# Optimization experiments

Hardware: AMD Instinct MI355X
Metric: run time of the kernel (lower is better)

## Reference

```python
import jax, jax.numpy as jnp
from jax import lax
import numpy as np

D_MODEL = 256
EXPAND = 2
D_INNER = D_MODEL * EXPAND
B, T = 8, 4096


def setup_inputs() -> dict:
    key = jax.random.key(0)
    ks = jax.random.split(key, 7)
    s_lin = 1.0 / np.sqrt(D_MODEL)
    s_gru_i = 1.0 / np.sqrt(D_MODEL)  # torch GRU init: U(-1/sqrt(hidden), 1/sqrt(hidden))
    x = jax.random.normal(ks[0], (B, T, D_MODEL), dtype=jnp.float32)
    W1 = jax.random.uniform(ks[1], (D_INNER, D_MODEL), jnp.float32, -s_lin, s_lin)
    b1 = jax.random.uniform(ks[2], (D_INNER,), jnp.float32, -s_lin, s_lin)
    W_ih = jax.random.uniform(ks[3], (3 * D_MODEL, D_INNER), jnp.float32, -s_gru_i, s_gru_i)
    b_ih = jax.random.uniform(ks[4], (3 * D_MODEL,), jnp.float32, -s_gru_i, s_gru_i)
    W_hh = jax.random.uniform(ks[5], (3 * D_MODEL, D_MODEL), jnp.float32, -s_gru_i, s_gru_i)
    b_hh = jax.random.uniform(ks[6], (3 * D_MODEL,), jnp.float32, -s_gru_i, s_gru_i)
    return {"x": x, "W1": W1, "b1": b1, "W_ih": W_ih, "b_ih": b_ih, "W_hh": W_hh, "b_hh": b_hh}


def reference(x, W1, b1, W_ih, b_ih, W_hh, b_hh):
    # Linear(d_model -> d_inner) + exact GELU (torch default)
    h = jax.nn.gelu(jnp.einsum('btd,id->bti', x, W1) + b1, approximate=False)  # [B,T,Di]
    Bb, Tt, _ = h.shape
    H = W_hh.shape[1]
    # Precompute input-side gate pre-activations for all timesteps (order: r, z, n)
    gx = jnp.einsum('bti,gi->btg', h, W_ih) + b_ih  # [B,T,3H]
    gx = jnp.moveaxis(gx, 1, 0)                     # [T,B,3H]

    def step(hprev, g):
        gh = hprev @ W_hh.T + b_hh                  # [B,3H]
        xr, xz, xn = jnp.split(g, 3, axis=-1)
        hr, hz, hn = jnp.split(gh, 3, axis=-1)
        r = jax.nn.sigmoid(xr + hr)
        z = jax.nn.sigmoid(xz + hz)
        n = jnp.tanh(xn + r * hn)
        hnew = (1.0 - z) * n + z * hprev
        return hnew, hnew

    h0 = jnp.zeros((Bb, H), dtype=x.dtype)
    _, out = lax.scan(step, h0, gx)                 # out: [T,B,H]
    return jnp.moveaxis(out, 0, 1)                  # [B,T,H]
```

## Files before the change

kernel.cpp:

```cpp
#include <hip/hip_runtime.h>
#include <hip/hip_fp16.h>
#include <hip/hip_bf16.h>

#define DM   256
#define DI   512
#define TG   768
#define TSEQ 4096
#define NB   8
#define MTOT (NB*TSEQ)

typedef _Float16 h2f __attribute__((ext_vector_type(2)));
typedef _Float16 h8f __attribute__((ext_vector_type(8)));

template<bool A_HALF, bool GELU_ACT>
__global__ __launch_bounds__(256) void gemm_bias(
    const void* __restrict__ Ap, const float* __restrict__ W,
    const float* __restrict__ bias, __half* __restrict__ C,
    int M, int N, int K)
{
  __shared__ float As[16][132];
  __shared__ float Ws[16][132];
  const int tid = threadIdx.x;
  const int tx = tid & 15, ty = tid >> 4;
  const int m0 = blockIdx.y * 128;
  const int n0 = blockIdx.x * 128;

  float acc[8][8] = {};

  for (int k0 = 0; k0 < K; k0 += 16) {
    if constexpr (A_HALF) {
      const __half* A = (const __half*)Ap;
      int r = tid >> 1, seg = (tid & 1) * 8;
      float4 raw = *(const float4*)(A + (size_t)(m0 + r) * K + k0 + seg);
      const __half* hv = (const __half*)&raw;
      #pragma unroll
      for (int q = 0; q < 8; q++) As[seg + q][r] = __half2float(hv[q]);
    } else {
      const float* A = (const float*)Ap;
      #pragma unroll
      for (int rep = 0; rep < 2; rep++) {
        int r = (tid >> 2) + rep * 64;
        int seg = (tid & 3) * 4;
        float4 v = *(const float4*)(A + (size_t)(m0 + r) * K + k0 + seg);
        As[seg + 0][r] = v.x; As[seg + 1][r] = v.y;
        As[seg + 2][r] = v.z; As[seg + 3][r] = v.w;
      }
    }
    #pragma unroll
    for (int rep = 0; rep < 2; rep++) {
      int r = (tid >> 2) + rep * 64;
      int seg = (tid & 3) * 4;
      float4 v = *(const float4*)(W + (size_t)(n0 + r) * K + k0 + seg);
      Ws[seg + 0][r] = v.x; Ws[seg + 1][r] = v.y;
      Ws[seg + 2][r] = v.z; Ws[seg + 3][r] = v.w;
    }
    __syncthreads();
    #pragma unroll
    for (int kk = 0; kk < 16; ++kk) {
      float a[8], b[8];
      *(float4*)&a[0] = *(const float4*)&As[kk][ty * 8];
      *(float4*)&a[4] = *(const float4*)&As[kk][ty * 8 + 4];
      *(float4*)&b[0] = *(const float4*)&Ws[kk][tx * 8];
      *(float4*)&b[4] = *(const float4*)&Ws[kk][tx * 8 + 4];
      #pragma unroll
      for (int i = 0; i < 8; i++)
        #pragma unroll
        for (int j = 0; j < 8; j++)
          acc[i][j] += a[i] * b[j];
    }
    __syncthreads();
  }

  #pragma unroll
  for (int i = 0; i < 8; i++) {
    int m = m0 + ty * 8 + i;
    #pragma unroll
    for (int j = 0; j < 8; j++) {
      int n = n0 + tx * 8 + j;
      float v = acc[i][j] + bias[n];
      if constexpr (GELU_ACT) {
        v = 0.5f * v * (1.0f + erff(v * 0.70710678118654752f));
      }
      C[(size_t)m * N + n] = __float2half(v);
    }
  }
}

__global__ __launch_bounds__(768, 3) void gru_scan(
    const __half* __restrict__ gx,
    const float*  __restrict__ Whh,
    const float*  __restrict__ bhh,
    float* __restrict__ out)
{
  const int b = blockIdx.x;
  const int j = threadIdx.x;

  __shared__ __align__(16) _Float16 h16[DM];
  __shared__ float gsig[2 * DM];

  h2f w[128];
  const float* wrow = Whh + (size_t)j * DM;
  #pragma unroll
  for (int k4 = 0; k4 < 64; k4++) {
    float4 f = ((const float4*)wrow)[k4];
    h2f t0; t0[0] = (_Float16)f.x; t0[1] = (_Float16)f.y;
    h2f t1; t1[0] = (_Float16)f.z; t1[1] = (_Float16)f.w;
    w[2 * k4]     = t0;
    w[2 * k4 + 1] = t1;
  }
  const float bias = bhh[j];
  float hloc = 0.0f;

  if (j < DM) h16[j] = (_Float16)0.0f;
  __syncthreads();

  const __half* gxb = gx + (size_t)b * TSEQ * TG;
  float* outb = out + (size_t)b * TSEQ * DM;

  float gxv = __half2float(gxb[j]);

  for (int t = 0; t < TSEQ; ++t) {
    float a0 = bias, a1 = 0.f, a2 = 0.f, a3 = 0.f;
    const h8f* hp8 = (const h8f*)h16;
    #pragma unroll
    for (int k = 0; k < 32; k++) {
      union { h8f v; h2f p[4]; } u;
      u.v = hp8[k];
      a0 = __builtin_amdgcn_fdot2(w[4 * k + 0], u.p[0], a0, false);
      a1 = __builtin_amdgcn_fdot2(w[4 * k + 1], u.p[1], a1, false);
      a2 = __builtin_amdgcn_fdot2(w[4 * k + 2], u.p[2], a2, false);
      a3 = __builtin_amdgcn_fdot2(w[4 * k + 3], u.p[3], a3, false);
    }
    float gh = (a0 + a1) + (a2 + a3);

    float gxn = 0.f;
    if (t + 1 < TSEQ) gxn = __half2float(gxb[(size_t)(t + 1) * TG + j]);

    if (j < 2 * DM) {
      float s = 1.0f / (1.0f + __expf(-(gxv + gh)));
      gsig[j] = s;
    }
    __syncthreads();
    if (j >= 2 * DM) {
      const int i = j - 2 * DM;
      float r = gsig[i];
      float z = gsig[i + DM];
      float n = tanhf(gxv + r * gh);
      float hn = (1.0f - z) * n + z * hloc;
      hloc = hn;
      h16[i] = (_Float16)hn;
      outb[(size_t)t * DM + i] = hn;
    }
    __syncthreads();
    gxv = gxn;
  }
}

extern "C" void kernel_launch(void* const* d_in, const int* in_sizes, int n_in,
                              void* d_out, int out_size, void* d_ws, size_t ws_size,
                              hipStream_t stream) {
  const float* x   = (const float*)d_in[0];
  const float* W1  = (const float*)d_in[1];
  const float* b1  = (const float*)d_in[2];
  const float* Wih = (const float*)d_in[3];
  const float* bih = (const float*)d_in[4];
  const float* Whh = (const float*)d_in[5];
  const float* bhh = (const float*)d_in[6];
  float* out = (float*)d_out;

  char* ws = (char*)d_ws;
  __half* h  = (__half*)ws;
  size_t h_bytes = (size_t)MTOT * DI * sizeof(__half);
  h_bytes = (h_bytes + 255) & ~(size_t)255;
  __half* gxbuf = (__half*)(ws + h_bytes);

  dim3 blk(256);
  gemm_bias<false, true><<<dim3(DI / 128, MTOT / 128), blk, 0, stream>>>(
      x, W1, b1, h, MTOT, DI, DM);
  gemm_bias<true, false><<<dim3(TG / 128, MTOT / 128), blk, 0, stream>>>(
      h, Wih, bih, gxbuf, MTOT, TG, DI);
  gru_scan<<<NB, 768, 0, stream>>>(gxbuf, Whh, bhh, out);
}
```

Baseline: 5.861 ms.

## Split GRU recurrent matvec across 4-lane groups with DPP reductions

Each group of four threads now shares four W_hh rows, and each thread covers a quarter of the K dimension for all four rows, combining partial sums with DPP xor-1/xor-2 butterfly adds. Each thread then picks out the reduced value for its own row. The aim is to cut per-thread LDS reads of the hidden state by a factor of four, since each thread now reads only 64 of the 256 h values. The cost is extra DPP and select instructions, plus sched_barriers that constrain instruction scheduling.

```diff
diff --git a/kernel.cpp b/kernel.cpp
--- a/kernel.cpp
+++ b/kernel.cpp
@@ -86,27 +86,51 @@
   }
 }
 
+__device__ __forceinline__ float dpp_xor1_add(float v) {
+  int i = __builtin_bit_cast(int, v);
+  int s = __builtin_amdgcn_update_dpp(i, i, 0xB1, 0xF, 0xF, true);
+  return v + __builtin_bit_cast(float, s);
+}
+__device__ __forceinline__ float dpp_xor2_add(float v) {
+  int i = __builtin_bit_cast(int, v);
+  int s = __builtin_amdgcn_update_dpp(i, i, 0x4E, 0xF, 0xF, true);
+  return v + __builtin_bit_cast(float, s);
+}
+
 __global__ __launch_bounds__(768, 3) void gru_scan(
     const __half* __restrict__ gx,
     const float*  __restrict__ Whh,
     const float*  __restrict__ bhh,
     float* __restrict__ out)
 {
-  const int b = blockIdx.x;
-  const int j = threadIdx.x;
+  const int b  = blockIdx.x;
+  const int j  = threadIdx.x;
+  const int g  = j >> 2;
+  const int q  = j & 3;
+  const int row0 = g << 2;
 
   __shared__ __align__(16) _Float16 h16[DM];
   __shared__ float gsig[2 * DM];
 
   h2f w[128];
-  const float* wrow = Whh + (size_t)j * DM;
   #pragma unroll
-  for (int k4 = 0; k4 < 64; k4++) {
-    float4 f = ((const float4*)wrow)[k4];
-    h2f t0; t0[0] = (_Float16)f.x; t0[1] = (_Float16)f.y;
-    h2f t1; t1[0] = (_Float16)f.z; t1[1] = (_Float16)f.w;
-    w[2 * k4]     = t0;
-    w[2 * k4 + 1] = t1;
+  for (int r = 0; r < 4; ++r) {
+    const float* wrow = Whh + (size_t)(row0 + r) * DM;
+    #pragma unroll
+    for (int i = 0; i < 8; ++i) {
+      const float* p = wrow + 8 * (q + 4 * i);
+      float4 f0 = *(const float4*)(p);
+      float4 f1 = *(const float4*)(p + 4);
+      h2f t0; t0[0] = (_Float16)f0.x; t0[1] = (_Float16)f0.y;
+      h2f t1; t1[0] = (_Float16)f0.z; t1[1] = (_Float16)f0.w;
+      h2f t2; t2[0] = (_Float16)f1.x; t2[1] = (_Float16)f1.y;
+      h2f t3; t3[0] = (_Float16)f1.z; t3[1] = (_Float16)f1.w;
+      w[r * 32 + 4 * i + 0] = t0;
+      w[r * 32 + 4 * i + 1] = t1;
+      w[r * 32 + 4 * i + 2] = t2;
+      w[r * 32 + 4 * i + 3] = t3;
+      __builtin_amdgcn_sched_barrier(0);
+    }
   }
   const float bias = bhh[j];
   float hloc = 0.0f;
@@ -114,42 +138,60 @@
   if (j < DM) h16[j] = (_Float16)0.0f;
   __syncthreads();
 
-  const __half* gxb = gx + (size_t)b * TSEQ * TG;
+  const __half* gxb = gx + (size_t)b * TSEQ * TG + j;
   float* outb = out + (size_t)b * TSEQ * DM;
 
-  float gxv = __half2float(gxb[j]);
+  float gxv = __half2float(gxb[0]);
+  const h8f* hp8 = (const h8f*)h16;
 
   for (int t = 0; t < TSEQ; ++t) {
-    float a0 = bias, a1 = 0.f, a2 = 0.f, a3 = 0.f;
-    const h8f* hp8 = (const h8f*)h16;
-    #pragma unroll
-    for (int k = 0; k < 32; k++) {
+    float a0 = 0.f, a1 = 0.f, a2 = 0.f, a3 = 0.f;
+    #pragma unroll
+    for (int i = 0; i < 8; ++i) {
       union { h8f v; h2f p[4]; } u;
-      u.v = hp8[k];
-      a0 = __builtin_amdgcn_fdot2(w[4 * k + 0], u.p[0], a0, false);
-      a1 = __builtin_amdgcn_fdot2(w[4 * k + 1], u.p[1], a1, false);
-      a2 = __builtin_amdgcn_fdot2(w[4 * k + 2], u.p[2], a2, false);
-      a3 = __builtin_amdgcn_fdot2(w[4 * k + 3], u.p[3], a3, false);
-    }
-    float gh = (a0 + a1) + (a2 + a3);
+      u.v = hp8[q + 4 * i];
+      a0 = __builtin_amdgcn_fdot2(w[      4 * i + 0], u.p[0], a0, false);
+      a0 = __builtin_amdgcn_fdot2(w[      4 * i + 1], u.p[1], a0, false);
+      a0 = __builtin_amdgcn_fdot2(w[      4 * i + 2], u.p[2], a0, false);
+      a0 = __builtin_amdgcn_fdot2(w[      4 * i + 3], u.p[3], a0, false);
+      a1 = __builtin_amdgcn_fdot2(w[ 32 + 4 * i + 0], u.p[0], a1, false);
+      a1 = __builtin_amdgcn_fdot2(w[ 32 + 4 * i + 1], u.p[1], a1, false);
+      a1 = __builtin_amdgcn_fdot2(w[ 32 + 4 * i + 2], u.p[2], a1, false);
+      a1 = __builtin_amdgcn_fdot2(w[ 32 + 4 * i + 3], u.p[3], a1, false);
+      a2 = __builtin_amdgcn_fdot2(w[ 64 + 4 * i + 0], u.p[0], a2, false);
+      a2 = __builtin_amdgcn_fdot2(w[ 64 + 4 * i + 1], u.p[1], a2, false);
+      a2 = __builtin_amdgcn_fdot2(w[ 64 + 4 * i + 2], u.p[2], a2, false);
+      a2 = __builtin_amdgcn_fdot2(w[ 64 + 4 * i + 3], u.p[3], a2, false);
+      a3 = __builtin_amdgcn_fdot2(w[ 96 + 4 * i + 0], u.p[0], a3, false);
+      a3 = __builtin_amdgcn_fdot2(w[ 96 + 4 * i + 1], u.p[1], a3, false);
+      a3 = __builtin_amdgcn_fdot2(w[ 96 + 4 * i + 2], u.p[2], a3, false);
+      a3 = __builtin_amdgcn_fdot2(w[ 96 + 4 * i + 3], u.p[3], a3, false);
+      if (i & 1) __builtin_amdgcn_sched_barrier(0);
+    }
+    a0 = dpp_xor2_add(dpp_xor1_add(a0));
+    a1 = dpp_xor2_add(dpp_xor1_add(a1));
+    a2 = dpp_xor2_add(dpp_xor1_add(a2));
+    a3 = dpp_xor2_add(dpp_xor1_add(a3));
+    float lo = (q & 1) ? a1 : a0;
+    float hi = (q & 1) ? a3 : a2;
+    float gh = ((q & 2) ? hi : lo) + bias;
 
     float gxn = 0.f;
-    if (t + 1 < TSEQ) gxn = __half2float(gxb[(size_t)(t + 1) * TG + j]);
+    if (t + 1 < TSEQ) gxn = __half2float(gxb[(size_t)(t + 1) * TG]);
 
     if (j < 2 * DM) {
-      float s = 1.0f / (1.0f + __expf(-(gxv + gh)));
-      gsig[j] = s;
+      gsig[j] = 1.0f / (1.0f + __expf(-(gxv + gh)));
     }
     __syncthreads();
     if (j >= 2 * DM) {
-      const int i = j - 2 * DM;
-      float r = gsig[i];
-      float z = gsig[i + DM];
+      const int i2 = j - 2 * DM;
+      float r = gsig[i2];
+      float z = gsig[i2 + DM];
       float n = tanhf(gxv + r * gh);
       float hn = (1.0f - z) * n + z * hloc;
       hloc = hn;
-      h16[i] = (_Float16)hn;
-      outb[(size_t)t * DM + i] = hn;
+      h16[i2] = (_Float16)hn;
+      outb[(size_t)t * DM + i2] = hn;
     }
     __syncthreads();
     gxv = gxn;
```

Result: faster. 5.600 ms (-4.4%).

## Restructure GRU scan so each thread pair computes all gates for one unit

Applied to the files above, without the earlier changes.

The recurrent scan now uses 512 threads in which a pair of lanes splits the K dimension for one hidden unit and computes the r, z and n dot products together. The two halves are combined with a DPP xor-1 add. Because all gate math stays in registers, the gsig shared-memory exchange goes away, and double-buffering the hidden state cuts the per-step barriers from two to one. The cost is 192 half2 weight registers per thread, which raises register pressure.

```diff
diff --git a/kernel.cpp b/kernel.cpp
--- a/kernel.cpp
+++ b/kernel.cpp
@@ -86,7 +86,13 @@
   }
 }
 
-__global__ __launch_bounds__(768, 3) void gru_scan(
+__device__ __forceinline__ float dpp_xor1_add(float v) {
+  int i = __builtin_bit_cast(int, v);
+  int s = __builtin_amdgcn_update_dpp(i, i, 0xB1, 0xF, 0xF, true);
+  return v + __builtin_bit_cast(float, s);
+}
+
+__global__ __launch_bounds__(512, 2) void gru_scan(
     const __half* __restrict__ gx,
     const float*  __restrict__ Whh,
     const float*  __restrict__ bhh,
@@ -94,65 +100,105 @@
 {
   const int b = blockIdx.x;
   const int j = threadIdx.x;
-
-  __shared__ __align__(16) _Float16 h16[DM];
-  __shared__ float gsig[2 * DM];
-
-  h2f w[128];
-  const float* wrow = Whh + (size_t)j * DM;
-  #pragma unroll
-  for (int k4 = 0; k4 < 64; k4++) {
-    float4 f = ((const float4*)wrow)[k4];
-    h2f t0; t0[0] = (_Float16)f.x; t0[1] = (_Float16)f.y;
-    h2f t1; t1[0] = (_Float16)f.z; t1[1] = (_Float16)f.w;
-    w[2 * k4]     = t0;
-    w[2 * k4 + 1] = t1;
-  }
-  const float bias = bhh[j];
+  const int u = j >> 1;
+  const int p = j & 1;
+
+  __shared__ __align__(16) _Float16 hbuf[2][DM];
+
+  h2f wr[64], wz[64], wn[64];
+  {
+    const float* rr = Whh + (size_t)u * DM + p * 128;
+    const float* rz = rr + (size_t)DM * DM;
+    const float* rn = rz + (size_t)DM * DM;
+    #pragma unroll
+    for (int i = 0; i < 32; ++i) {
+      float4 f = *(const float4*)(rr + 4 * i);
+      h2f t0; t0[0] = (_Float16)f.x; t0[1] = (_Float16)f.y;
+      h2f t1; t1[0] = (_Float16)f.z; t1[1] = (_Float16)f.w;
+      wr[2 * i] = t0; wr[2 * i + 1] = t1;
+      if (i & 1) __builtin_amdgcn_sched_barrier(0);
+    }
+    #pragma unroll
+    for (int i = 0; i < 32; ++i) {
+      float4 f = *(const float4*)(rz + 4 * i);
+      h2f t0; t0[0] = (_Float16)f.x; t0[1] = (_Float16)f.y;
+      h2f t1; t1[0] = (_Float16)f.z; t1[1] = (_Float16)f.w;
+      wz[2 * i] = t0; wz[2 * i + 1] = t1;
+      if (i & 1) __builtin_amdgcn_sched_barrier(0);
+    }
+    #pragma unroll
+    for (int i = 0; i < 32; ++i) {
+      float4 f = *(const float4*)(rn + 4 * i);
+      h2f t0; t0[0] = (_Float16)f.x; t0[1] = (_Float16)f.y;
+      h2f t1; t1[0] = (_Float16)f.z; t1[1] = (_Float16)f.w;
+      wn[2 * i] = t0; wn[2 * i + 1] = t1;
+      if (i & 1) __builtin_amdgcn_sched_barrier(0);
+    }
+  }
+  const float br = bhh[u];
+  const float bz = bhh[DM + u];
+  const float bn = bhh[2 * DM + u];
   float hloc = 0.0f;
 
-  if (j < DM) h16[j] = (_Float16)0.0f;
+  if (j < DM) hbuf[0][j] = (_Float16)0.0f;
   __syncthreads();
 
-  const __half* gxb = gx + (size_t)b * TSEQ * TG;
+  const __half* gp = gx + (size_t)b * TSEQ * TG;
   float* outb = out + (size_t)b * TSEQ * DM;
 
-  float gxv = __half2float(gxb[j]);
+  float gxr = __half2float(gp[u]);
+  float gxz = __half2float(gp[DM + u]);
+  float gxn = __half2float(gp[2 * DM + u]);
 
   for (int t = 0; t < TSEQ; ++t) {
-    float a0 = bias, a1 = 0.f, a2 = 0.f, a3 = 0.f;
-    const h8f* hp8 = (const h8f*)h16;
-    #pragma unroll
-    for (int k = 0; k < 32; k++) {
-      union { h8f v; h2f p[4]; } u;
-      u.v = hp8[k];
-      a0 = __builtin_amdgcn_fdot2(w[4 * k + 0], u.p[0], a0, false);
-      a1 = __builtin_amdgcn_fdot2(w[4 * k + 1], u.p[1], a1, false);
-      a2 = __builtin_amdgcn_fdot2(w[4 * k + 2], u.p[2], a2, false);
-      a3 = __builtin_amdgcn_fdot2(w[4 * k + 3], u.p[3], a3, false);
-    }
-    float gh = (a0 + a1) + (a2 + a3);
-
-    float gxn = 0.f;
-    if (t + 1 < TSEQ) gxn = __half2float(gxb[(size_t)(t + 1) * TG + j]);
-
-    if (j < 2 * DM) {
-      float s = 1.0f / (1.0f + __expf(-(gxv + gh)));
-      gsig[j] = s;
+    const int cur = t & 1;
+    const h8f* hp = (const h8f*)(&hbuf[cur][0]) + p * 16;
+
+    float nr = 0.f, nz = 0.f, nn = 0.f;
+    if (t + 1 < TSEQ) {
+      const __half* g1 = gp + TG;
+      nr = __half2float(g1[u]);
+      nz = __half2float(g1[DM + u]);
+      nn = __half2float(g1[2 * DM + u]);
+    }
+
+    float ar = 0.f, az = 0.f, an = 0.f;
+    #pragma unroll
+    for (int i = 0; i < 16; ++i) {
+      union { h8f v; h2f c[4]; } hh;
+      hh.v = hp[i];
+      ar = __builtin_amdgcn_fdot2(wr[4 * i + 0], hh.c[0], ar, false);
+      az = __builtin_amdgcn_fdot2(wz[4 * i + 0], hh.c[0], az, false);
+      an = __builtin_amdgcn_fdot2(wn[4 * i + 0], hh.c[0], an, false);
+      ar = __builtin_amdgcn_fdot2(wr[4 * i + 1], hh.c[1], ar, false);
+      az = __builtin_amdgcn_fdot2(wz[4 * i + 1], hh.c[1], az, false);
+      an = __builtin_amdgcn_fdot2(wn[4 * i + 1], hh.c[1], an, false);
+      ar = __builtin_amdgcn_fdot2(wr[4 * i + 2], hh.c[2], ar, false);
+      az = __builtin_amdgcn_fdot2(wz[4 * i + 2], hh.c[2], az, false);
+      an = __builtin_amdgcn_fdot2(wn[4 * i + 2], hh.c[2], an, false);
+      ar = __builtin_amdgcn_fdot2(wr[4 * i + 3], hh.c[3], ar, false);
+      az = __builtin_amdgcn_fdot2(wz[4 * i + 3], hh.c[3], az, false);
+      an = __builtin_amdgcn_fdot2(wn[4 * i + 3], hh.c[3], an, false);
+      if (i & 1) __builtin_amdgcn_sched_barrier(0);
+    }
+    ar = dpp_xor1_add(ar);
+    az = dpp_xor1_add(az);
+    an = dpp_xor1_add(an);
+
+    float r = 1.0f / (1.0f + __expf(-(gxr + ar + br)));
+    float z = 1.0f / (1.0f + __expf(-(gxz + az + bz)));
+    float n = tanhf(gxn + r * (an + bn));
+    float hnew = (1.0f - z) * n + z * hloc;
+    hloc = hnew;
+
+    if (p == 0) {
+      hbuf[cur ^ 1][u] = (_Float16)hnew;
+      outb[(size_t)t * DM + u] = hnew;
     }
     __syncthreads();
-    if (j >= 2 * DM) {
-      const int i = j - 2 * DM;
-      float r = gsig[i];
-      float z = gsig[i + DM];
-      float n = tanhf(gxv + r * gh);
-      float hn = (1.0f - z) * n + z * hloc;
-      hloc = hn;
-      h16[i] = (_Float16)hn;
-      outb[(size_t)t * DM + i] = hn;
-    }
-    __syncthreads();
-    gxv = gxn;
+
+    gp += TG;
+    gxr = nr; gxz = nz; gxn = nn;
   }
 }
 
@@ -179,5 +225,5 @@
       x, W1, b1, h, MTOT, DI, DM);
   gemm_bias<true, false><<<dim3(TG / 128, MTOT / 128), blk, 0, stream>>>(
       h, Wih, bih, gxbuf, MTOT, TG, DI);
-  gru_scan<<<NB, 768, 0, stream>>>(gxbuf, Whh, bhh, out);
-}
+  gru_scan<<<NB, 512, 0, stream>>>(gxbuf, Whh, bhh, out);
+}
```

New measurement: 5.879 ms. About the same (+0.3%).
